# Performance work log

Measured on AMD Instinct MI355X. Metric: run time of the kernel, lower is better.

The kernel has to match this reference:

```python
import jax, jax.numpy as jnp
import numpy as np

IN_FEATURES = 4096
OUT_FEATURES = 4096
M_TOKENS = 8192
WEIGHT_SCALE = 0.1
OUT_SCALE = 0.1


def setup_inputs() -> dict:
    key = jax.random.key(0)
    k_x, k_w = jax.random.split(key)
    # int8-valued activations and weights in [-128, 128), stored as int32 carriers
    x_q = jax.random.randint(k_x, (M_TOKENS, IN_FEATURES), 0, 256, dtype=jnp.int32) - 128
    weight_q = jax.random.randint(k_w, (OUT_FEATURES, IN_FEATURES), 0, 256, dtype=jnp.int32) - 128
    scale_x = jnp.float32(0.05)
    return {"x_q": x_q, "weight_q": weight_q, "scale_x": scale_x}


def reference(x_q, weight_q, scale_x):
    acc = jnp.einsum("mk,nk->mn", x_q.astype(jnp.int32), weight_q.astype(jnp.int32))
    # fused epilogue: rescale, round-to-nearest, saturate to int8
    scale = scale_x * jnp.float32(WEIGHT_SCALE) / jnp.float32(OUT_SCALE)
    y = acc.astype(jnp.float32) * scale
    y_q = jnp.clip(jnp.round(y), -128.0, 127.0).astype(jnp.int8)
    return (y_q, jnp.float32(OUT_SCALE))
```

## Files before the change

### kernel.cpp

```cpp
#include <hip/hip_runtime.h>
#include <stdint.h>

typedef int v4i  __attribute__((ext_vector_type(4)));
typedef int v16i __attribute__((ext_vector_type(16)));

#define M_TOK 8192
#define N_OUT 4096
#define K_IN  4096

__device__ __forceinline__ int pack4(int4 a) {
    return (a.x & 255) | ((a.y & 255) << 8) | ((a.z & 255) << 16) | ((a.w & 255) << 24);
}

__global__ __launch_bounds__(256) void pack_kernel(
    const int4* __restrict__ x, const int* __restrict__ w,
    int* __restrict__ dA, int4* __restrict__ dBp, int n4x, int nB16)
{
    int i = blockIdx.x * blockDim.x + threadIdx.x;
    if (i < n4x) {
        dA[i] = pack4(x[i]);
    } else {
        int t = i - n4x;
        if (t < nB16) {
            int lane = t & 63;
            int c    = (t >> 6) & 127;
            int n32  = t >> 13;
            int row  = n32 * 32 + (lane & 31);
            int col  = c * 32 + (lane >> 5) * 16;
            const int4* src = (const int4*)(w + (size_t)row * K_IN + col);
            int4 p;
            p.x = pack4(src[0]);
            p.y = pack4(src[1]);
            p.z = pack4(src[2]);
            p.w = pack4(src[3]);
            dBp[t] = p;
        }
    }
}

__global__ __launch_bounds__(256) void gemm_i8_kernel(
    const char* __restrict__ A8,
    const int*  __restrict__ Bp,
    const float* __restrict__ scale_ptr,
    float* __restrict__ out)
{
    __shared__ alignas(16) char lA[2][128 * 128];

    const int tid  = threadIdx.x;
    const int wave = tid >> 6;
    const int lane = tid & 63;

    const int bm = blockIdx.x * 128;
    const int bn = blockIdx.y * 128;

    const int wm = (wave >> 1) * 64;
    const int wn = (wave & 1) * 64;

    v16i acc[2][2];
#pragma unroll
    for (int i = 0; i < 2; ++i)
#pragma unroll
        for (int j = 0; j < 2; ++j)
#pragma unroll
            for (int r = 0; r < 16; ++r)
                acc[i][j][r] = 0;

    const int srow = lane >> 3;
    const int scol = ((lane & 7) ^ srow) << 4;

    const char* gA[4];
    char* lp0[4];
    char* lp1[4];
#pragma unroll
    for (int q = 0; q < 4; ++q) {
        int row0 = wave * 32 + q * 8;
        gA[q]  = A8 + (size_t)(bm + row0 + srow) * K_IN + scol;
        lp0[q] = lA[0] + row0 * 128;
        lp1[q] = lA[1] + row0 * 128;
    }

    const v4i* Bb = (const v4i*)Bp + (size_t)((bn >> 5) + (wn >> 5)) * (128 * 64) + lane;

    const int fm  = lane & 31;
    const int fh  = lane >> 5;
    const int fsw = fm & 7;

    v4i b0[8], b1[8];

#pragma unroll
    for (int t = 0; t < 2; ++t)
#pragma unroll
        for (int kk = 0; kk < 4; ++kk)
            b0[t * 4 + kk] = Bb[(size_t)(t * 128 + kk) * 64];
#pragma unroll
    for (int q = 0; q < 4; ++q)
        __builtin_amdgcn_global_load_lds(
            (const __attribute__((address_space(1))) void*)(gA[q]),
            (__attribute__((address_space(3))) void*)lp0[q], 16, 0, 0);
    __syncthreads();

#pragma unroll 1
    for (int k0 = 0; k0 < K_IN; k0 += 256) {
        {
            const int kn = (k0 + 128) & (K_IN - 1);
            const int cn = kn >> 5;
#pragma unroll
            for (int t = 0; t < 2; ++t)
#pragma unroll
                for (int kk = 0; kk < 4; ++kk)
                    b1[t * 4 + kk] = Bb[(size_t)(t * 128 + cn + kk) * 64];
#pragma unroll
            for (int q = 0; q < 4; ++q)
                __builtin_amdgcn_global_load_lds(
                    (const __attribute__((address_space(1))) void*)(gA[q] + kn),
                    (__attribute__((address_space(3))) void*)lp1[q], 16, 0, 0);
#pragma unroll
            for (int kk = 0; kk < 4; ++kk) {
                const int goff = ((kk * 2 + fh) ^ fsw) << 4;
                v4i af0 = *(const v4i*)(lA[0] + (wm + fm) * 128 + goff);
                v4i af1 = *(const v4i*)(lA[0] + (wm + 32 + fm) * 128 + goff);
                acc[0][0] = __builtin_amdgcn_mfma_i32_32x32x32_i8(af0, b0[kk],     acc[0][0], 0, 0, 0);
                acc[0][1] = __builtin_amdgcn_mfma_i32_32x32x32_i8(af0, b0[4 + kk], acc[0][1], 0, 0, 0);
                acc[1][0] = __builtin_amdgcn_mfma_i32_32x32x32_i8(af1, b0[kk],     acc[1][0], 0, 0, 0);
                acc[1][1] = __builtin_amdgcn_mfma_i32_32x32x32_i8(af1, b0[4 + kk], acc[1][1], 0, 0, 0);
            }
            __syncthreads();
        }
        {
            const int kn = (k0 + 256) & (K_IN - 1);
            const int cn = kn >> 5;
#pragma unroll
            for (int t = 0; t < 2; ++t)
#pragma unroll
                for (int kk = 0; kk < 4; ++kk)
                    b0[t * 4 + kk] = Bb[(size_t)(t * 128 + cn + kk) * 64];
#pragma unroll
            for (int q = 0; q < 4; ++q)
                __builtin_amdgcn_global_load_lds(
                    (const __attribute__((address_space(1))) void*)(gA[q] + kn),
                    (__attribute__((address_space(3))) void*)lp0[q], 16, 0, 0);
#pragma unroll
            for (int kk = 0; kk < 4; ++kk) {
                const int goff = ((kk * 2 + fh) ^ fsw) << 4;
                v4i af0 = *(const v4i*)(lA[1] + (wm + fm) * 128 + goff);
                v4i af1 = *(const v4i*)(lA[1] + (wm + 32 + fm) * 128 + goff);
                acc[0][0] = __builtin_amdgcn_mfma_i32_32x32x32_i8(af0, b1[kk],     acc[0][0], 0, 0, 0);
                acc[0][1] = __builtin_amdgcn_mfma_i32_32x32x32_i8(af0, b1[4 + kk], acc[0][1], 0, 0, 0);
                acc[1][0] = __builtin_amdgcn_mfma_i32_32x32x32_i8(af1, b1[kk],     acc[1][0], 0, 0, 0);
                acc[1][1] = __builtin_amdgcn_mfma_i32_32x32x32_i8(af1, b1[4 + kk], acc[1][1], 0, 0, 0);
            }
            __syncthreads();
        }
    }

    const float s     = scale_ptr[0];
    const float scale = (s * 0.1f) / 0.1f;

#pragma unroll
    for (int ti = 0; ti < 2; ++ti) {
#pragma unroll
        for (int tj = 0; tj < 2; ++tj) {
#pragma unroll
            for (int r = 0; r < 16; ++r) {
                int row = bm + wm + ti * 32 + (r & 3) + 8 * (r >> 2) + 4 * fh;
                int col = bn + wn + tj * 32 + fm;
                float y = (float)acc[ti][tj][r] * scale;
                y = rintf(y);
                y = fminf(fmaxf(y, -128.0f), 127.0f);
                out[(size_t)row * N_OUT + col] = y;
            }
        }
    }

    if (bm == 0 && bn == 0 && tid == 0)
        out[(size_t)M_TOK * N_OUT] = 0.1f;
}

extern "C" void kernel_launch(void* const* d_in, const int* in_sizes, int n_in,
                              void* d_out, int out_size, void* d_ws, size_t ws_size,
                              hipStream_t stream)
{
    const int*   x_q     = (const int*)d_in[0];
    const int*   w_q     = (const int*)d_in[1];
    const float* scale_x = (const float*)d_in[2];
    float* out = (float*)d_out;

    char* A8 = (char*)d_ws;
    char* Bp = (char*)d_ws + (size_t)M_TOK * K_IN;

    const int n4x  = (M_TOK * K_IN) / 4;
    const int nB16 = (N_OUT * K_IN) / 16;

    pack_kernel<<<(n4x + nB16 + 255) / 256, 256, 0, stream>>>(
        (const int4*)x_q, w_q, (int*)A8, (int4*)Bp, n4x, nB16);

    dim3 grid(M_TOK / 128, N_OUT / 128);
    gemm_i8_kernel<<<grid, 256, 0, stream>>>(A8, (const int*)Bp, scale_x, out);
}
```

Measured before the change: 418.3 us.

## Widen GEMM block tile to 128x256 with 64x128 per-wave tiles

Doubles the N extent of each workgroup and each wave, so every wave keeps eight 32x32 accumulators and each A fragment read from LDS feeds four MFMAs instead of two. This halves A reloads per output and the grid size. The B register double-buffer is dropped: B fragments are now loaded at the top of each 128-wide K step instead of prefetched a step ahead, which may expose global load latency. Register pressure rises (128 accumulator VGPRs), and launch_bounds(256,2) is added to cap occupancy.

```diff
diff --git a/kernel.cpp b/kernel.cpp
--- a/kernel.cpp
+++ b/kernel.cpp
@@ -27,18 +27,18 @@
             int n32  = t >> 13;
             int row  = n32 * 32 + (lane & 31);
             int col  = c * 32 + (lane >> 5) * 16;
-            const int4* src = (const int4*)(w + (size_t)row * K_IN + col);
+            const int4* s = (const int4*)(w + (size_t)row * K_IN + col);
             int4 p;
-            p.x = pack4(src[0]);
-            p.y = pack4(src[1]);
-            p.z = pack4(src[2]);
-            p.w = pack4(src[3]);
+            p.x = pack4(s[0]);
+            p.y = pack4(s[1]);
+            p.z = pack4(s[2]);
+            p.w = pack4(s[3]);
             dBp[t] = p;
         }
     }
 }
 
-__global__ __launch_bounds__(256) void gemm_i8_kernel(
+__global__ __launch_bounds__(256, 2) void gemm_i8_kernel(
     const char* __restrict__ A8,
     const int*  __restrict__ Bp,
     const float* __restrict__ scale_ptr,
@@ -51,16 +51,16 @@
     const int lane = tid & 63;
 
     const int bm = blockIdx.x * 128;
-    const int bn = blockIdx.y * 128;
+    const int bn = blockIdx.y * 256;
 
     const int wm = (wave >> 1) * 64;
-    const int wn = (wave & 1) * 64;
+    const int wn = (wave & 1) * 128;
 
-    v16i acc[2][2];
+    v16i acc[2][4];
 #pragma unroll
     for (int i = 0; i < 2; ++i)
 #pragma unroll
-        for (int j = 0; j < 2; ++j)
+        for (int j = 0; j < 4; ++j)
 #pragma unroll
             for (int r = 0; r < 16; ++r)
                 acc[i][j][r] = 0;
@@ -69,89 +69,63 @@
     const int scol = ((lane & 7) ^ srow) << 4;
 
     const char* gA[4];
-    char* lp0[4];
-    char* lp1[4];
+    char* lAp[2][4];
 #pragma unroll
     for (int q = 0; q < 4; ++q) {
         int row0 = wave * 32 + q * 8;
-        gA[q]  = A8 + (size_t)(bm + row0 + srow) * K_IN + scol;
-        lp0[q] = lA[0] + row0 * 128;
-        lp1[q] = lA[1] + row0 * 128;
+        gA[q]     = A8 + (size_t)(bm + row0 + srow) * K_IN + scol;
+        lAp[0][q] = lA[0] + row0 * 128;
+        lAp[1][q] = lA[1] + row0 * 128;
     }
 
-    const v4i* Bb = (const v4i*)Bp + (size_t)((bn >> 5) + (wn >> 5)) * (128 * 64) + lane;
+    const v4i* Bb = (const v4i*)Bp + (size_t)((bn + wn) >> 5) * (128 * 64) + lane;
 
     const int fm  = lane & 31;
     const int fh  = lane >> 5;
     const int fsw = fm & 7;
 
-    v4i b0[8], b1[8];
+#define STAGE_A(koff, buf)                                                    \
+    {                                                                         \
+        _Pragma("unroll")                                                     \
+        for (int q = 0; q < 4; ++q)                                           \
+            __builtin_amdgcn_global_load_lds(                                 \
+                (const __attribute__((address_space(1))) void*)(gA[q] + (koff)), \
+                (__attribute__((address_space(3))) void*)lAp[buf][q], 16, 0, 0); \
+    }
 
-#pragma unroll
-    for (int t = 0; t < 2; ++t)
-#pragma unroll
-        for (int kk = 0; kk < 4; ++kk)
-            b0[t * 4 + kk] = Bb[(size_t)(t * 128 + kk) * 64];
-#pragma unroll
-    for (int q = 0; q < 4; ++q)
-        __builtin_amdgcn_global_load_lds(
-            (const __attribute__((address_space(1))) void*)(gA[q]),
-            (__attribute__((address_space(3))) void*)lp0[q], 16, 0, 0);
+    STAGE_A(0, 0);
     __syncthreads();
 
 #pragma unroll 1
-    for (int k0 = 0; k0 < K_IN; k0 += 256) {
-        {
-            const int kn = (k0 + 128) & (K_IN - 1);
-            const int cn = kn >> 5;
+    for (int k0 = 0; k0 < K_IN; k0 += 128) {
+        const int cur = (k0 >> 7) & 1;
+        const int c0  = k0 >> 5;
+
+        v4i bf[4][4];
 #pragma unroll
-            for (int t = 0; t < 2; ++t)
+        for (int kk = 0; kk < 4; ++kk)
 #pragma unroll
-                for (int kk = 0; kk < 4; ++kk)
-                    b1[t * 4 + kk] = Bb[(size_t)(t * 128 + cn + kk) * 64];
+            for (int t = 0; t < 4; ++t)
+                bf[kk][t] = Bb[(size_t)(t * 128 + c0 + kk) * 64];
+
+        if (k0 + 128 < K_IN) STAGE_A(k0 + 128, cur ^ 1);
+
 #pragma unroll
-            for (int q = 0; q < 4; ++q)
-                __builtin_amdgcn_global_load_lds(
-                    (const __attribute__((address_space(1))) void*)(gA[q] + kn),
-                    (__attribute__((address_space(3))) void*)lp1[q], 16, 0, 0);
+        for (int kk = 0; kk < 4; ++kk) {
+            const int goff = ((kk * 2 + fh) ^ fsw) << 4;
+            v4i af0 = *(const v4i*)(lA[cur] + (wm + fm) * 128 + goff);
+            v4i af1 = *(const v4i*)(lA[cur] + (wm + 32 + fm) * 128 + goff);
 #pragma unroll
-            for (int kk = 0; kk < 4; ++kk) {
-                const int goff = ((kk * 2 + fh) ^ fsw) << 4;
-                v4i af0 = *(const v4i*)(lA[0] + (wm + fm) * 128 + goff);
-                v4i af1 = *(const v4i*)(lA[0] + (wm + 32 + fm) * 128 + goff);
-                acc[0][0] = __builtin_amdgcn_mfma_i32_32x32x32_i8(af0, b0[kk],     acc[0][0], 0, 0, 0);
-                acc[0][1] = __builtin_amdgcn_mfma_i32_32x32x32_i8(af0, b0[4 + kk], acc[0][1], 0, 0, 0);
-                acc[1][0] = __builtin_amdgcn_mfma_i32_32x32x32_i8(af1, b0[kk],     acc[1][0], 0, 0, 0);
-                acc[1][1] = __builtin_amdgcn_mfma_i32_32x32x32_i8(af1, b0[4 + kk], acc[1][1], 0, 0, 0);
+            for (int t = 0; t < 4; ++t) {
+                acc[0][t] = __builtin_amdgcn_mfma_i32_32x32x32_i8(af0, bf[kk][t], acc[0][t], 0, 0, 0);
+                acc[1][t] = __builtin_amdgcn_mfma_i32_32x32x32_i8(af1, bf[kk][t], acc[1][t], 0, 0, 0);
             }
-            __syncthreads();
         }
-        {
-            const int kn = (k0 + 256) & (K_IN - 1);
-            const int cn = kn >> 5;
-#pragma unroll
-            for (int t = 0; t < 2; ++t)
-#pragma unroll
-                for (int kk = 0; kk < 4; ++kk)
-                    b0[t * 4 + kk] = Bb[(size_t)(t * 128 + cn + kk) * 64];
-#pragma unroll
-            for (int q = 0; q < 4; ++q)
-                __builtin_amdgcn_global_load_lds(
-                    (const __attribute__((address_space(1))) void*)(gA[q] + kn),
-                    (__attribute__((address_space(3))) void*)lp0[q], 16, 0, 0);
-#pragma unroll
-            for (int kk = 0; kk < 4; ++kk) {
-                const int goff = ((kk * 2 + fh) ^ fsw) << 4;
-                v4i af0 = *(const v4i*)(lA[1] + (wm + fm) * 128 + goff);
-                v4i af1 = *(const v4i*)(lA[1] + (wm + 32 + fm) * 128 + goff);
-                acc[0][0] = __builtin_amdgcn_mfma_i32_32x32x32_i8(af0, b1[kk],     acc[0][0], 0, 0, 0);
-                acc[0][1] = __builtin_amdgcn_mfma_i32_32x32x32_i8(af0, b1[4 + kk], acc[0][1], 0, 0, 0);
-                acc[1][0] = __builtin_amdgcn_mfma_i32_32x32x32_i8(af1, b1[kk],     acc[1][0], 0, 0, 0);
-                acc[1][1] = __builtin_amdgcn_mfma_i32_32x32x32_i8(af1, b1[4 + kk], acc[1][1], 0, 0, 0);
-            }
-            __syncthreads();
-        }
+
+        __syncthreads();
     }
+
+#undef STAGE_A
 
     const float s     = scale_ptr[0];
     const float scale = (s * 0.1f) / 0.1f;
@@ -159,7 +133,7 @@
 #pragma unroll
     for (int ti = 0; ti < 2; ++ti) {
 #pragma unroll
-        for (int tj = 0; tj < 2; ++tj) {
+        for (int tj = 0; tj < 4; ++tj) {
 #pragma unroll
             for (int r = 0; r < 16; ++r) {
                 int row = bm + wm + ti * 32 + (r & 3) + 8 * (r >> 2) + 4 * fh;
@@ -194,6 +168,7 @@
     pack_kernel<<<(n4x + nB16 + 255) / 256, 256, 0, stream>>>(
         (const int4*)x_q, w_q, (int*)A8, (int4*)Bp, n4x, nB16);
 
-    dim3 grid(M_TOK / 128, N_OUT / 128);
-    gemm_i8_kernel<<<grid, 256, 0, stream>>>(A8, (const int*)Bp, scale_x, out);
+    dim3 grid(M_TOK / 128, N_OUT / 256);
+    gemm_i8_kernel<<<grid, 256, 0, stream>>>(
+        A8, (const int*)Bp, scale_x, out);
 }
```

Result: faster. 405.5 us (-3.1%).
